# Optimization experiments

Measured on AMD Instinct MI355X. Metric: run time of the kernel, lower is better.

## Reference

```python
import jax, jax.numpy as jnp
import numpy as np
import math

B, C, HLAT, WLON = 1, 256, 46, 90
HEADS = 8
KC = 256   # k_channels (defaults to in_channels)
OC = 256   # out_channels (defaults to in_channels)


def _cc_weights(n):
    # Clenshaw-Curtis quadrature weights on n nodes x_k = cos(k*pi/(n-1)) over [-1, 1]
    # (torch-harmonics 'equiangular' grid quadrature); weights sum to 2.
    N = n - 1
    k = np.arange(n)
    j = np.arange(1, N // 2 + 1)
    b = np.where(2 * j == N, 1.0, 2.0)
    s = (b / (4.0 * j**2 - 1.0))[None, :] * np.cos(2.0 * np.pi * np.outer(k, j) / N)
    w = (1.0 - s.sum(axis=1)) * (2.0 / N)
    w[0] *= 0.5
    w[-1] *= 0.5
    return w


def _log_quad_weights(nlat, nlon):
    wgl = _cc_weights(nlat).astype(np.float32)            # [nlat]
    qw = 2.0 * np.pi * wgl / nlon                          # [nlat]
    qw = np.tile(qw.reshape(-1, 1), (1, nlon)).flatten()   # [nlat*nlon]
    return np.log(qw).reshape(1, 1, -1)                    # (1, 1, N)


def setup_inputs() -> dict:
    key = jax.random.key(0)
    ks = jax.random.split(key, 6)
    scale_qkv = math.sqrt(3.0 / C)
    scale_proj = math.sqrt(3.0 / OC)
    uni = lambda k, shp, s: s * (2.0 * jax.random.uniform(k, shp, dtype=jnp.float32) - 1.0)
    return {
        "query": jax.random.normal(ks[0], (B, C, HLAT, WLON), dtype=jnp.float32),
        "q_w": uni(ks[1], (KC, C), scale_qkv),
        "q_b": jnp.zeros((KC,), dtype=jnp.float32),
        "k_w": uni(ks[2], (KC, C), scale_qkv),
        "k_b": jnp.zeros((KC,), dtype=jnp.float32),
        "v_w": uni(ks[3], (OC, C), scale_qkv),
        "v_b": jnp.zeros((OC,), dtype=jnp.float32),
        "p_w": uni(ks[4], (OC, OC), scale_proj),
        "p_b": jnp.zeros((OC,), dtype=jnp.float32),
        "log_qw": jnp.asarray(_log_quad_weights(HLAT, WLON)),
    }


def _conv1x1(x, w, b):
    # 1x1 conv == per-pixel channel GEMM
    return jnp.einsum("bchw,kc->bkhw", x, w) + b[None, :, None, None]


def _to_seq(x, heads):
    # [B, heads*d, H, W] -> [B, heads, H*W, d]
    b, c, h, w = x.shape
    d = c // heads
    return x.reshape(b, heads, d, h, w).transpose(0, 1, 3, 4, 2).reshape(b, heads, h * w, d)


def reference(query, q_w, q_b, k_w, k_b, v_w, v_b, p_w, p_b, log_qw):
    # key = value = query (self-attention path of the module)
    q = _conv1x1(query, q_w, q_b)
    k = _conv1x1(query, k_w, k_b)
    v = _conv1x1(query, v_w, v_b)

    qs = _to_seq(q, HEADS)   # [B, h, N, dk]
    ks = _to_seq(k, HEADS)   # [B, h, M, dk]
    vs = _to_seq(v, HEADS)   # [B, h, M, dv]

    dk = KC // HEADS
    scale = 1.0 / math.sqrt(dk)  # SDPA default scale
    # scores with additive log-quadrature-weight bias over keys
    scores = jnp.einsum("bhnd,bhmd->bhnm", qs, ks) * scale + log_qw[:, :, None, :]
    attn = jax.nn.softmax(scores, axis=-1)
    out = jnp.einsum("bhnm,bhmd->bhnd", attn, vs)  # [B, h, N, dv]

    bb, hh, nn, dv = out.shape
    out = out.transpose(0, 1, 3, 2).reshape(bb, hh * dv, HLAT, WLON)
    out = _conv1x1(out, p_w, p_b)
    return out
```

## Files before the change

### kernel.cpp

```cpp
#include <hip/hip_runtime.h>

#define N_SEQ 4140
#define NP    4160
#define C_IN  256
#define HEADS 8
#define NT32  130
#define HN    (HEADS * N_SEQ)
#define LOG2E 1.4426950408889634f
#define SCALE2 (0.17677669529663687f * LOG2E)
#define INVSCALE 5.656854249492381f

typedef _Float16 f16x8 __attribute__((ext_vector_type(8)));
typedef float    f32x16 __attribute__((ext_vector_type(16)));

__device__ inline unsigned short f16b(float x) {
    union { _Float16 h; unsigned short s; } c;
    c.h = (_Float16)x;
    return c.s;
}
__device__ inline unsigned pack2h(float lo, float hi) {
    union { _Float16 h[2]; unsigned u; } c;
    c.h[0] = (_Float16)lo;
    c.h[1] = (_Float16)hi;
    return c.u;
}
__device__ inline void permswap(unsigned &a, unsigned &b) {
    asm volatile("v_permlane32_swap_b32 %0, %1" : "+v"(a), "+v"(b));
}

__global__ __launch_bounds__(256) void prep_kernel(
    const float* __restrict__ x, const float* __restrict__ log_qw,
    const float* __restrict__ q_w, const float* __restrict__ k_w,
    const float* __restrict__ v_w, const float* __restrict__ p_w,
    unsigned short* __restrict__ xt, float* __restrict__ lw2,
    unsigned short* __restrict__ wf, unsigned short* __restrict__ pwf)
{
    if (blockIdx.x < NT32) {
        __shared__ unsigned short tile[32][33];
        const int tx = threadIdx.x & 31, ty = threadIdx.x >> 5;
        const int n0 = blockIdx.x * 32, c0 = blockIdx.y * 32;
#pragma unroll
        for (int i = 0; i < 4; ++i) {
            const int c = c0 + ty * 4 + i;
            const int n = n0 + tx;
            const float v = (n < N_SEQ) ? x[(size_t)c * N_SEQ + n] : 0.f;
            tile[tx][ty * 4 + i] = f16b(v);
        }
        __syncthreads();
#pragma unroll
        for (int i = 0; i < 4; ++i) {
            const int nl = ty * 4 + i;
            xt[(size_t)(n0 + nl) * C_IN + c0 + tx] = tile[nl][tx];
        }
    } else {
        const int bid = (blockIdx.x - NT32) * 8 + blockIdx.y;
        for (int i = bid * 256 + threadIdx.x; i < 262144 + NP; i += 24 * 256) {
            if (i < 65536)        wf[i] = f16b(q_w[i]);
            else if (i < 131072)  wf[i] = f16b(k_w[i - 65536]);
            else if (i < 196608)  wf[i] = f16b(v_w[i - 131072]);
            else if (i < 262144)  pwf[i - 196608] = f16b(p_w[i - 196608]);
            else {
                const int j = i - 262144;
                lw2[j] = (j < N_SEQ) ? log_qw[j] * INVSCALE : -1e30f;
            }
        }
    }
}

__global__ __launch_bounds__(256) void qkv_mfma(
    const unsigned short* __restrict__ xt, const unsigned short* __restrict__ wf,
    const float* __restrict__ q_b, const float* __restrict__ k_b,
    const float* __restrict__ v_b,
    unsigned short* __restrict__ qo, unsigned short* __restrict__ ko,
    unsigned short* __restrict__ vo)
{
    const int tid = threadIdx.x, wid = tid >> 6, lane = tid & 63;
    const int col = lane & 31, hi = lane >> 5;
    const int w = blockIdx.x * 4 + wid;
    const int ot = w / 65, pt = w % 65;
    const int n0 = pt * 64, n1 = n0 + 32;

    if (ot < 16) {
        const unsigned short* a0 = xt + (size_t)(n0 + col) * C_IN + hi * 8;
        const unsigned short* a1 = xt + (size_t)(n1 + col) * C_IN + hi * 8;
        const unsigned short* bw = wf + (size_t)(ot * 32 + col) * C_IN + hi * 8;
        const float bias = (ot < 8) ? q_b[ot * 32 + col] : k_b[(ot - 8) * 32 + col];
        f32x16 acc0, acc1;
#pragma unroll
        for (int r = 0; r < 16; ++r) { acc0[r] = bias; acc1[r] = bias; }
#pragma unroll
        for (int t = 0; t < 16; ++t) {
            const f16x8 bf  = *(const f16x8*)(const void*)(bw + t * 16);
            const f16x8 af0 = *(const f16x8*)(const void*)(a0 + t * 16);
            const f16x8 af1 = *(const f16x8*)(const void*)(a1 + t * 16);
            acc0 = __builtin_amdgcn_mfma_f32_32x32x16_f16(af0, bf, acc0, 0, 0, 0);
            acc1 = __builtin_amdgcn_mfma_f32_32x32x16_f16(af1, bf, acc1, 0, 0, 0);
        }
        unsigned short* dst = (ot < 8) ? qo : ko;
        const int h = ot & 7;
#pragma unroll
        for (int r = 0; r < 16; ++r) {
            const int rl = (r & 3) + 8 * (r >> 2) + 4 * hi;
            dst[(size_t)(h * NP + n0 + rl) * 32 + col] = f16b(acc0[r]);
            dst[(size_t)(h * NP + n1 + rl) * 32 + col] = f16b(acc1[r]);
        }
    } else {
        const int h = ot - 16;
        const unsigned short* aw = wf + (size_t)(512 + h * 32 + col) * C_IN + hi * 8;
        const unsigned short* b0 = xt + (size_t)(n0 + col) * C_IN + hi * 8;
        const unsigned short* b1 = xt + (size_t)(n1 + col) * C_IN + hi * 8;
        const float* vb4 = v_b + h * 32 + 4 * hi;
        const float4 c0 = *(const float4*)(vb4);
        const float4 c1 = *(const float4*)(vb4 + 8);
        const float4 c2 = *(const float4*)(vb4 + 16);
        const float4 c3 = *(const float4*)(vb4 + 24);
        f32x16 acc0;
        acc0[0]=c0.x; acc0[1]=c0.y; acc0[2]=c0.z; acc0[3]=c0.w;
        acc0[4]=c1.x; acc0[5]=c1.y; acc0[6]=c1.z; acc0[7]=c1.w;
        acc0[8]=c2.x; acc0[9]=c2.y; acc0[10]=c2.z; acc0[11]=c2.w;
        acc0[12]=c3.x; acc0[13]=c3.y; acc0[14]=c3.z; acc0[15]=c3.w;
        f32x16 acc1 = acc0;
#pragma unroll
        for (int t = 0; t < 16; ++t) {
            const f16x8 af  = *(const f16x8*)(const void*)(aw + t * 16);
            const f16x8 bf0 = *(const f16x8*)(const void*)(b0 + t * 16);
            const f16x8 bf1 = *(const f16x8*)(const void*)(b1 + t * 16);
            acc0 = __builtin_amdgcn_mfma_f32_32x32x16_f16(af, bf0, acc0, 0, 0, 0);
            acc1 = __builtin_amdgcn_mfma_f32_32x32x16_f16(af, bf1, acc1, 0, 0, 0);
        }
        const int nt0 = pt * 2, nt1 = nt0 + 1;
#pragma unroll
        for (int r = 0; r < 16; ++r) {
            const int d = (r & 3) + 8 * (r >> 2) + 4 * hi;
            vo[((size_t)(h * NT32 + nt0) * 32 + d) * 32 + col] = f16b(acc0[r]);
            vo[((size_t)(h * NT32 + nt1) * 32 + d) * 32 + col] = f16b(acc1[r]);
        }
    }
}

__global__ __launch_bounds__(256) void attn_mfma_kernel(
    const unsigned short* __restrict__ qb, const unsigned short* __restrict__ kb,
    const unsigned short* __restrict__ vb, const float* __restrict__ lw2,
    float* __restrict__ pm, float* __restrict__ pl, float* __restrict__ pacc,
    int tiles_per_z)
{
    const int tid = threadIdx.x;
    const int wid = tid >> 6;
    const int lane = tid & 63;
    const int col = lane & 31;
    const int hi = lane >> 5;
    const int job = blockIdx.x * 4 + wid;
    const int h = job / 65;
    const int pt = job % 65;
    const int z = blockIdx.y;

    const int qrowA = pt * 64 + col;
    const int qrowB = qrowA + 32;
    const unsigned short* qpA = qb + ((size_t)(h * NP + qrowA)) * 32 + hi * 8;
    const unsigned short* qpB = qb + ((size_t)(h * NP + qrowB)) * 32 + hi * 8;
    const f16x8 qfA0 = *(const f16x8*)(const void*)(qpA);
    const f16x8 qfA1 = *(const f16x8*)(const void*)(qpA + 16);
    const f16x8 qfB0 = *(const f16x8*)(const void*)(qpB);
    const f16x8 qfB1 = *(const f16x8*)(const void*)(qpB + 16);

    f32x16 oA, oB;
#pragma unroll
    for (int r = 0; r < 16; ++r) { oA[r] = 0.f; oB[r] = 0.f; }
    float mA = -1e30f, lsA = 0.f;
    float mB = -1e30f, lsB = 0.f;

    const int t0 = z * tiles_per_z;
    const int t1 = min(NT32, t0 + tiles_per_z);
    const unsigned short* kbase = kb + (size_t)h * NP * 32;
    const unsigned short* vbase = vb + (size_t)h * NT32 * 1024;

    for (int t = t0; t < t1; ++t) {
        const int k0 = t * 32;
        const unsigned short* kp = kbase + (size_t)(k0 + col) * 32 + hi * 8;
        const f16x8 ka0 = *(const f16x8*)(const void*)(kp);
        const f16x8 ka1 = *(const f16x8*)(const void*)(kp + 16);
        const unsigned short* vp = vbase + (size_t)t * 1024 + col * 32 + hi * 8;
        const f16x8 va0 = *(const f16x8*)(const void*)(vp);
        const f16x8 va1 = *(const f16x8*)(const void*)(vp + 16);

        const float* lw4 = lw2 + k0 + 4 * hi;
        const float4 w0 = *(const float4*)(lw4);
        const float4 w1 = *(const float4*)(lw4 + 8);
        const float4 w2 = *(const float4*)(lw4 + 16);
        const float4 w3 = *(const float4*)(lw4 + 24);
        f32x16 sI;
        sI[0]=w0.x; sI[1]=w0.y; sI[2]=w0.z; sI[3]=w0.w;
        sI[4]=w1.x; sI[5]=w1.y; sI[6]=w1.z; sI[7]=w1.w;
        sI[8]=w2.x; sI[9]=w2.y; sI[10]=w2.z; sI[11]=w2.w;
        sI[12]=w3.x; sI[13]=w3.y; sI[14]=w3.z; sI[15]=w3.w;

        f32x16 sA = sI, sB = sI;
        sA = __builtin_amdgcn_mfma_f32_32x32x16_f16(ka0, qfA0, sA, 0, 0, 0);
        sB = __builtin_amdgcn_mfma_f32_32x32x16_f16(ka0, qfB0, sB, 0, 0, 0);
        sA = __builtin_amdgcn_mfma_f32_32x32x16_f16(ka1, qfA1, sA, 0, 0, 0);
        sB = __builtin_amdgcn_mfma_f32_32x32x16_f16(ka1, qfB1, sB, 0, 0, 0);

        float pA[16], pB[16];
#pragma unroll
        for (int r = 0; r < 16; ++r) { pA[r] = sA[r] * SCALE2; pB[r] = sB[r] * SCALE2; }

        float ax0 = fmaxf(pA[0], pA[1]),   ax1 = fmaxf(pA[2], pA[3]);
        float ax2 = fmaxf(pA[4], pA[5]),   ax3 = fmaxf(pA[6], pA[7]);
        float ax4 = fmaxf(pA[8], pA[9]),   ax5 = fmaxf(pA[10], pA[11]);
        float ax6 = fmaxf(pA[12], pA[13]), ax7 = fmaxf(pA[14], pA[15]);
        float bx0 = fmaxf(pB[0], pB[1]),   bx1 = fmaxf(pB[2], pB[3]);
        float bx2 = fmaxf(pB[4], pB[5]),   bx3 = fmaxf(pB[6], pB[7]);
        float bx4 = fmaxf(pB[8], pB[9]),   bx5 = fmaxf(pB[10], pB[11]);
        float bx6 = fmaxf(pB[12], pB[13]), bx7 = fmaxf(pB[14], pB[15]);
        ax0 = fmaxf(ax0, ax1); ax2 = fmaxf(ax2, ax3);
        ax4 = fmaxf(ax4, ax5); ax6 = fmaxf(ax6, ax7);
        bx0 = fmaxf(bx0, bx1); bx2 = fmaxf(bx2, bx3);
        bx4 = fmaxf(bx4, bx5); bx6 = fmaxf(bx6, bx7);
        const float cmaxA = fmaxf(fmaxf(ax0, ax2), fmaxf(ax4, ax6));
        const float cmaxB = fmaxf(fmaxf(bx0, bx2), fmaxf(bx4, bx6));

        if (!__all(cmaxA - mA <= 8.0f)) {
            float cw = fmaxf(cmaxA, __shfl_xor(cmaxA, 32));
            const float mnew = fmaxf(mA, cw);
            const float esc = __builtin_amdgcn_exp2f(mA - mnew);
            lsA *= esc;
#pragma unroll
            for (int r = 0; r < 16; ++r) oA[r] *= esc;
            mA = mnew;
        }
        if (!__all(cmaxB - mB <= 8.0f)) {
            float cw = fmaxf(cmaxB, __shfl_xor(cmaxB, 32));
            const float mnew = fmaxf(mB, cw);
            const float esc = __builtin_amdgcn_exp2f(mB - mnew);
            lsB *= esc;
#pragma unroll
            for (int r = 0; r < 16; ++r) oB[r] *= esc;
            mB = mnew;
        }

#pragma unroll
        for (int r = 0; r < 16; ++r) {
            pA[r] = __builtin_amdgcn_exp2f(pA[r] - mA);
            pB[r] = __builtin_amdgcn_exp2f(pB[r] - mB);
        }
        {
            float s0 = (pA[0] + pA[1]) + (pA[2] + pA[3]);
            float s1 = (pA[4] + pA[5]) + (pA[6] + pA[7]);
            float s2 = (pA[8] + pA[9]) + (pA[10] + pA[11]);
            float s3 = (pA[12] + pA[13]) + (pA[14] + pA[15]);
            lsA += (s0 + s1) + (s2 + s3);
            float u0 = (pB[0] + pB[1]) + (pB[2] + pB[3]);
            float u1 = (pB[4] + pB[5]) + (pB[6] + pB[7]);
            float u2 = (pB[8] + pB[9]) + (pB[10] + pB[11]);
            float u3 = (pB[12] + pB[13]) + (pB[14] + pB[15]);
            lsB += (u0 + u1) + (u2 + u3);
        }

        union U { unsigned u[4]; f16x8 v; };
        {
            unsigned a0 = pack2h(pA[0], pA[1]),  b0 = pack2h(pA[2], pA[3]);
            unsigned c0 = pack2h(pA[4], pA[5]),  d0 = pack2h(pA[6], pA[7]);
            permswap(a0, c0); permswap(b0, d0);
            U pb0; pb0.u[0]=a0; pb0.u[1]=b0; pb0.u[2]=c0; pb0.u[3]=d0;
            oA = __builtin_amdgcn_mfma_f32_32x32x16_f16(va0, pb0.v, oA, 0, 0, 0);
            unsigned e0 = pack2h(pA[8], pA[9]),   f0 = pack2h(pA[10], pA[11]);
            unsigned g0 = pack2h(pA[12], pA[13]), h0 = pack2h(pA[14], pA[15]);
            permswap(e0, g0); permswap(f0, h0);
            U pb1; pb1.u[0]=e0; pb1.u[1]=f0; pb1.u[2]=g0; pb1.u[3]=h0;
            oA = __builtin_amdgcn_mfma_f32_32x32x16_f16(va1, pb1.v, oA, 0, 0, 0);
        }
        {
            unsigned a0 = pack2h(pB[0], pB[1]),  b0 = pack2h(pB[2], pB[3]);
            unsigned c0 = pack2h(pB[4], pB[5]),  d0 = pack2h(pB[6], pB[7]);
            permswap(a0, c0); permswap(b0, d0);
            U pb0; pb0.u[0]=a0; pb0.u[1]=b0; pb0.u[2]=c0; pb0.u[3]=d0;
            oB = __builtin_amdgcn_mfma_f32_32x32x16_f16(va0, pb0.v, oB, 0, 0, 0);
            unsigned e0 = pack2h(pB[8], pB[9]),   f0 = pack2h(pB[10], pB[11]);
            unsigned g0 = pack2h(pB[12], pB[13]), h0 = pack2h(pB[14], pB[15]);
            permswap(e0, g0); permswap(f0, h0);
            U pb1; pb1.u[0]=e0; pb1.u[1]=f0; pb1.u[2]=g0; pb1.u[3]=h0;
            oB = __builtin_amdgcn_mfma_f32_32x32x16_f16(va1, pb1.v, oB, 0, 0, 0);
        }
    }

    lsA += __shfl_xor(lsA, 32);
    lsB += __shfl_xor(lsB, 32);

    if (qrowA < N_SEQ) {
        const size_t qi = (size_t)h * N_SEQ + qrowA;
        if (hi == 0) {
            pm[(size_t)z * HN + qi] = mA;
            pl[(size_t)z * HN + qi] = lsA;
        }
        float* pa = pacc + ((size_t)z * HN + qi) * 32;
#pragma unroll
        for (int r = 0; r < 16; ++r)
            pa[(r & 3) + 8 * (r >> 2) + 4 * hi] = oA[r];
    }
    if (qrowB < N_SEQ) {
        const size_t qi = (size_t)h * N_SEQ + qrowB;
        if (hi == 0) {
            pm[(size_t)z * HN + qi] = mB;
            pl[(size_t)z * HN + qi] = lsB;
        }
        float* pa = pacc + ((size_t)z * HN + qi) * 32;
#pragma unroll
        for (int r = 0; r < 16; ++r)
            pa[(r & 3) + 8 * (r >> 2) + 4 * hi] = oB[r];
    }
}

__global__ __launch_bounds__(256) void merge_kernel(
    const float* __restrict__ pm, const float* __restrict__ pl,
    const float* __restrict__ pacc, unsigned short* __restrict__ at_t, int nz)
{
    const int idx = blockIdx.x * 256 + threadIdx.x;
    if (idx >= HN) return;
    const int h = idx / N_SEQ;
    const int n = idx - h * N_SEQ;

    float mg = pm[idx];
    for (int zz = 1; zz < nz; ++zz) mg = fmaxf(mg, pm[(size_t)zz * HN + idx]);

    float lg = 0.f;
    float acc[32];
#pragma unroll
    for (int d = 0; d < 32; ++d) acc[d] = 0.f;
    for (int zz = 0; zz < nz; ++zz) {
        const float e = exp2f(pm[(size_t)zz * HN + idx] - mg);
        lg += pl[(size_t)zz * HN + idx] * e;
        const float* pa = pacc + ((size_t)zz * HN + idx) * 32;
#pragma unroll
        for (int d = 0; d < 32; ++d) acc[d] = fmaf(pa[d], e, acc[d]);
    }
    const float inv = 1.0f / lg;
    union { unsigned short s[32]; uint4 u[4]; } ph;
#pragma unroll
    for (int d = 0; d < 32; ++d) ph.s[d] = f16b(acc[d] * inv);
    uint4* dst = (uint4*)(at_t + (size_t)n * C_IN + h * 32);
#pragma unroll
    for (int i = 0; i < 4; ++i) dst[i] = ph.u[i];
}

__global__ __launch_bounds__(256) void proj_mfma(
    const unsigned short* __restrict__ at_t, const unsigned short* __restrict__ pwf,
    const float* __restrict__ p_b, float* __restrict__ out)
{
    const int tid = threadIdx.x, wid = tid >> 6, lane = tid & 63;
    const int col = lane & 31, hi = lane >> 5;
    const int tile = blockIdx.x * 4 + wid;
    const int ot = tile / NT32, nt = tile % NT32;
    const int n0 = nt * 32;

    const unsigned short* arow = pwf + (size_t)(ot * 32 + col) * C_IN + hi * 8;
    const unsigned short* brow = at_t + (size_t)(n0 + col) * C_IN + hi * 8;

    const float* pb4 = p_b + ot * 32 + 4 * hi;
    const float4 c0 = *(const float4*)(pb4);
    const float4 c1 = *(const float4*)(pb4 + 8);
    const float4 c2 = *(const float4*)(pb4 + 16);
    const float4 c3 = *(const float4*)(pb4 + 24);
    f32x16 acca, accb;
    acca[0]=c0.x; acca[1]=c0.y; acca[2]=c0.z; acca[3]=c0.w;
    acca[4]=c1.x; acca[5]=c1.y; acca[6]=c1.z; acca[7]=c1.w;
    acca[8]=c2.x; acca[9]=c2.y; acca[10]=c2.z; acca[11]=c2.w;
    acca[12]=c3.x; acca[13]=c3.y; acca[14]=c3.z; acca[15]=c3.w;
#pragma unroll
    for (int r = 0; r < 16; ++r) accb[r] = 0.f;

#pragma unroll
    for (int t = 0; t < 8; ++t) {
        const f16x8 afa = *(const f16x8*)(const void*)(arow + t * 16);
        const f16x8 bfa = *(const f16x8*)(const void*)(brow + t * 16);
        const f16x8 afb = *(const f16x8*)(const void*)(arow + (t + 8) * 16);
        const f16x8 bfb = *(const f16x8*)(const void*)(brow + (t + 8) * 16);
        acca = __builtin_amdgcn_mfma_f32_32x32x16_f16(afa, bfa, acca, 0, 0, 0);
        accb = __builtin_amdgcn_mfma_f32_32x32x16_f16(afb, bfb, accb, 0, 0, 0);
    }

    const int n = n0 + col;
    if (n < N_SEQ) {
#pragma unroll
        for (int r = 0; r < 16; ++r) {
            const int oc = ot * 32 + (r & 3) + 8 * (r >> 2) + 4 * hi;
            out[(size_t)oc * N_SEQ + n] = acca[r] + accb[r];
        }
    }
}

extern "C" void kernel_launch(void* const* d_in, const int* in_sizes, int n_in,
                              void* d_out, int out_size, void* d_ws, size_t ws_size,
                              hipStream_t stream) {
    const float* query  = (const float*)d_in[0];
    const float* q_w    = (const float*)d_in[1];
    const float* q_b    = (const float*)d_in[2];
    const float* k_w    = (const float*)d_in[3];
    const float* k_b    = (const float*)d_in[4];
    const float* v_w    = (const float*)d_in[5];
    const float* v_b    = (const float*)d_in[6];
    const float* p_w    = (const float*)d_in[7];
    const float* p_b    = (const float*)d_in[8];
    const float* log_qw = (const float*)d_in[9];

    const size_t HNP32 = (size_t)HEADS * NP * 32;

    unsigned short* xt  = (unsigned short*)d_ws;
    unsigned short* qb  = xt + (size_t)NP * C_IN;
    unsigned short* kb  = qb + HNP32;
    unsigned short* vb  = kb + HNP32;
    unsigned short* wf  = vb + HNP32;
    unsigned short* pwf = wf + 768 * 256;
    float* lw2 = (float*)(pwf + 256 * 256);
    float* pm  = lw2 + NP;
    unsigned short* at_t = qb;

    const size_t base_bytes = (size_t)((char*)pm - (char*)d_ws);
    const size_t per_z = (size_t)HN * 34 * sizeof(float);
    int nz = 1;
    if      (ws_size >= base_bytes + 4 * per_z) nz = 4;
    else if (ws_size >= base_bytes + 2 * per_z) nz = 2;
    const int tiles_per_z = (NT32 + nz - 1) / nz;

    float* pl   = pm + (size_t)nz * HN;
    float* pacc = pl + (size_t)nz * HN;

    prep_kernel<<<dim3(NT32 + 3, 8), 256, 0, stream>>>(
        query, log_qw, q_w, k_w, v_w, p_w, xt, lw2, wf, pwf);

    qkv_mfma<<<dim3(390), 256, 0, stream>>>(
        xt, wf, q_b, k_b, v_b, qb, kb, vb);

    attn_mfma_kernel<<<dim3(130, nz), 256, 0, stream>>>(
        qb, kb, vb, lw2, pm, pl, pacc, tiles_per_z);

    merge_kernel<<<dim3((HN + 255) / 256), 256, 0, stream>>>(
        pm, pl, pacc, at_t, nz);

    proj_mfma<<<dim3(260), 256, 0, stream>>>(
        at_t, pwf, p_b, (float*)d_out);
}
```

Baseline: 181.0 us.

## Fold softmax scale into Q weights, use packed f16 convert and dot2 row sums

Pre-multiplies the Q projection weights and bias by the log2-scaled softmax factor and stores the bias as log_qw*LOG2E, which removes the per-element score scaling in the attention inner loop. Converts probabilities with cvt_pkrtz and computes row sums with fdot2 on the packed f16 values, replacing separate float adds and per-half conversions. Also allows an 8-way key split when the workspace is large enough, giving more blocks in exchange for a larger merge step. Row sums now come from round-toward-zero f16 values, which slightly changes precision.

Result: faster. 171.6 us (-5.2%).

```diff
diff --git a/kernel.cpp b/kernel.cpp
--- a/kernel.cpp
+++ b/kernel.cpp
@@ -8,9 +8,9 @@
 #define HN    (HEADS * N_SEQ)
 #define LOG2E 1.4426950408889634f
 #define SCALE2 (0.17677669529663687f * LOG2E)
-#define INVSCALE 5.656854249492381f
 
 typedef _Float16 f16x8 __attribute__((ext_vector_type(8)));
+typedef _Float16 f16x2 __attribute__((ext_vector_type(2)));
 typedef float    f32x16 __attribute__((ext_vector_type(16)));
 
 __device__ inline unsigned short f16b(float x) {
@@ -18,11 +18,11 @@
     c.h = (_Float16)x;
     return c.s;
 }
-__device__ inline unsigned pack2h(float lo, float hi) {
-    union { _Float16 h[2]; unsigned u; } c;
-    c.h[0] = (_Float16)lo;
-    c.h[1] = (_Float16)hi;
-    return c.u;
+__device__ inline f16x2 pkrtz(float a, float b) {
+    auto r = __builtin_amdgcn_cvt_pkrtz(a, b);
+    union { decltype(r) i; f16x2 o; } c;
+    c.i = r;
+    return c.o;
 }
 __device__ inline void permswap(unsigned &a, unsigned &b) {
     asm volatile("v_permlane32_swap_b32 %0, %1" : "+v"(a), "+v"(b));
@@ -55,13 +55,13 @@
     } else {
         const int bid = (blockIdx.x - NT32) * 8 + blockIdx.y;
         for (int i = bid * 256 + threadIdx.x; i < 262144 + NP; i += 24 * 256) {
-            if (i < 65536)        wf[i] = f16b(q_w[i]);
+            if (i < 65536)        wf[i] = f16b(q_w[i] * SCALE2);
             else if (i < 131072)  wf[i] = f16b(k_w[i - 65536]);
             else if (i < 196608)  wf[i] = f16b(v_w[i - 131072]);
             else if (i < 262144)  pwf[i - 196608] = f16b(p_w[i - 196608]);
             else {
                 const int j = i - 262144;
-                lw2[j] = (j < N_SEQ) ? log_qw[j] * INVSCALE : -1e30f;
+                lw2[j] = (j < N_SEQ) ? log_qw[j] * LOG2E : -1e30f;
             }
         }
     }
@@ -84,7 +84,8 @@
         const unsigned short* a0 = xt + (size_t)(n0 + col) * C_IN + hi * 8;
         const unsigned short* a1 = xt + (size_t)(n1 + col) * C_IN + hi * 8;
         const unsigned short* bw = wf + (size_t)(ot * 32 + col) * C_IN + hi * 8;
-        const float bias = (ot < 8) ? q_b[ot * 32 + col] : k_b[(ot - 8) * 32 + col];
+        const float bias = (ot < 8) ? q_b[ot * 32 + col] * SCALE2
+                                    : k_b[(ot - 8) * 32 + col];
         f32x16 acc0, acc1;
 #pragma unroll
         for (int r = 0; r < 16; ++r) { acc0[r] = bias; acc1[r] = bias; }
@@ -168,6 +169,7 @@
     for (int r = 0; r < 16; ++r) { oA[r] = 0.f; oB[r] = 0.f; }
     float mA = -1e30f, lsA = 0.f;
     float mB = -1e30f, lsB = 0.f;
+    const f16x2 one2 = { (_Float16)1.f, (_Float16)1.f };
 
     const int t0 = z * tiles_per_z;
     const int t1 = min(NT32, t0 + tiles_per_z);
@@ -188,36 +190,32 @@
         const float4 w1 = *(const float4*)(lw4 + 8);
         const float4 w2 = *(const float4*)(lw4 + 16);
         const float4 w3 = *(const float4*)(lw4 + 24);
-        f32x16 sI;
-        sI[0]=w0.x; sI[1]=w0.y; sI[2]=w0.z; sI[3]=w0.w;
-        sI[4]=w1.x; sI[5]=w1.y; sI[6]=w1.z; sI[7]=w1.w;
-        sI[8]=w2.x; sI[9]=w2.y; sI[10]=w2.z; sI[11]=w2.w;
-        sI[12]=w3.x; sI[13]=w3.y; sI[14]=w3.z; sI[15]=w3.w;
-
-        f32x16 sA = sI, sB = sI;
+        f32x16 sA;
+        sA[0]=w0.x; sA[1]=w0.y; sA[2]=w0.z; sA[3]=w0.w;
+        sA[4]=w1.x; sA[5]=w1.y; sA[6]=w1.z; sA[7]=w1.w;
+        sA[8]=w2.x; sA[9]=w2.y; sA[10]=w2.z; sA[11]=w2.w;
+        sA[12]=w3.x; sA[13]=w3.y; sA[14]=w3.z; sA[15]=w3.w;
+        f32x16 sB = sA;
+
         sA = __builtin_amdgcn_mfma_f32_32x32x16_f16(ka0, qfA0, sA, 0, 0, 0);
         sB = __builtin_amdgcn_mfma_f32_32x32x16_f16(ka0, qfB0, sB, 0, 0, 0);
         sA = __builtin_amdgcn_mfma_f32_32x32x16_f16(ka1, qfA1, sA, 0, 0, 0);
         sB = __builtin_amdgcn_mfma_f32_32x32x16_f16(ka1, qfB1, sB, 0, 0, 0);
 
-        float pA[16], pB[16];
-#pragma unroll
-        for (int r = 0; r < 16; ++r) { pA[r] = sA[r] * SCALE2; pB[r] = sB[r] * SCALE2; }
-
-        float ax0 = fmaxf(pA[0], pA[1]),   ax1 = fmaxf(pA[2], pA[3]);
-        float ax2 = fmaxf(pA[4], pA[5]),   ax3 = fmaxf(pA[6], pA[7]);
-        float ax4 = fmaxf(pA[8], pA[9]),   ax5 = fmaxf(pA[10], pA[11]);
-        float ax6 = fmaxf(pA[12], pA[13]), ax7 = fmaxf(pA[14], pA[15]);
-        float bx0 = fmaxf(pB[0], pB[1]),   bx1 = fmaxf(pB[2], pB[3]);
-        float bx2 = fmaxf(pB[4], pB[5]),   bx3 = fmaxf(pB[6], pB[7]);
-        float bx4 = fmaxf(pB[8], pB[9]),   bx5 = fmaxf(pB[10], pB[11]);
-        float bx6 = fmaxf(pB[12], pB[13]), bx7 = fmaxf(pB[14], pB[15]);
-        ax0 = fmaxf(ax0, ax1); ax2 = fmaxf(ax2, ax3);
-        ax4 = fmaxf(ax4, ax5); ax6 = fmaxf(ax6, ax7);
-        bx0 = fmaxf(bx0, bx1); bx2 = fmaxf(bx2, bx3);
-        bx4 = fmaxf(bx4, bx5); bx6 = fmaxf(bx6, bx7);
-        const float cmaxA = fmaxf(fmaxf(ax0, ax2), fmaxf(ax4, ax6));
-        const float cmaxB = fmaxf(fmaxf(bx0, bx2), fmaxf(bx4, bx6));
+        const float a0m = fmaxf(fmaxf(sA[0], sA[1]), sA[2]);
+        const float a1m = fmaxf(fmaxf(sA[3], sA[4]), sA[5]);
+        const float a2m = fmaxf(fmaxf(sA[6], sA[7]), sA[8]);
+        const float a3m = fmaxf(fmaxf(sA[9], sA[10]), sA[11]);
+        const float a4m = fmaxf(fmaxf(sA[12], sA[13]), sA[14]);
+        const float cmaxA = fmaxf(fmaxf(fmaxf(a0m, a1m), a2m),
+                                  fmaxf(fmaxf(a3m, a4m), sA[15]));
+        const float b0m = fmaxf(fmaxf(sB[0], sB[1]), sB[2]);
+        const float b1m = fmaxf(fmaxf(sB[3], sB[4]), sB[5]);
+        const float b2m = fmaxf(fmaxf(sB[6], sB[7]), sB[8]);
+        const float b3m = fmaxf(fmaxf(sB[9], sB[10]), sB[11]);
+        const float b4m = fmaxf(fmaxf(sB[12], sB[13]), sB[14]);
+        const float cmaxB = fmaxf(fmaxf(fmaxf(b0m, b1m), b2m),
+                                  fmaxf(fmaxf(b3m, b4m), sB[15]));
 
         if (!__all(cmaxA - mA <= 8.0f)) {
             float cw = fmaxf(cmaxA, __shfl_xor(cmaxA, 32));
@@ -238,48 +236,65 @@
             mB = mnew;
         }
 
+        float pA[16], pB[16];
 #pragma unroll
         for (int r = 0; r < 16; ++r) {
-            pA[r] = __builtin_amdgcn_exp2f(pA[r] - mA);
-            pB[r] = __builtin_amdgcn_exp2f(pB[r] - mB);
-        }
+            pA[r] = __builtin_amdgcn_exp2f(sA[r] - mA);
+            pB[r] = __builtin_amdgcn_exp2f(sB[r] - mB);
+        }
+
+        union PK { f16x2 h[4]; unsigned u[4]; f16x8 v; };
         {
-            float s0 = (pA[0] + pA[1]) + (pA[2] + pA[3]);
-            float s1 = (pA[4] + pA[5]) + (pA[6] + pA[7]);
-            float s2 = (pA[8] + pA[9]) + (pA[10] + pA[11]);
-            float s3 = (pA[12] + pA[13]) + (pA[14] + pA[15]);
-            lsA += (s0 + s1) + (s2 + s3);
-            float u0 = (pB[0] + pB[1]) + (pB[2] + pB[3]);
-            float u1 = (pB[4] + pB[5]) + (pB[6] + pB[7]);
-            float u2 = (pB[8] + pB[9]) + (pB[10] + pB[11]);
-            float u3 = (pB[12] + pB[13]) + (pB[14] + pB[15]);
-            lsB += (u0 + u1) + (u2 + u3);
-        }
-
-        union U { unsigned u[4]; f16x8 v; };
+            PK k0p, k1p;
+            k0p.h[0] = pkrtz(pA[0], pA[1]);
+            k0p.h[1] = pkrtz(pA[2], pA[3]);
+            k0p.h[2] = pkrtz(pA[4], pA[5]);
+            k0p.h[3] = pkrtz(pA[6], pA[7]);
+            k1p.h[0] = pkrtz(pA[8], pA[9]);
+            k1p.h[1] = pkrtz(pA[10], pA[11]);
+            k1p.h[2] = pkrtz(pA[12], pA[13]);
+            k1p.h[3] = pkrtz(pA[14], pA[15]);
+            float sa = __builtin_amdgcn_fdot2(k0p.h[0], one2, 0.f, false);
+            float sb = __builtin_amdgcn_fdot2(k0p.h[1], one2, 0.f, false);
+            sa = __builtin_amdgcn_fdot2(k0p.h[2], one2, sa, false);
+            sb = __builtin_amdgcn_fdot2(k0p.h[3], one2, sb, false);
+            sa = __builtin_amdgcn_fdot2(k1p.h[0], one2, sa, false);
+            sb = __builtin_amdgcn_fdot2(k1p.h[1], one2, sb, false);
+            sa = __builtin_amdgcn_fdot2(k1p.h[2], one2, sa, false);
+            sb = __builtin_amdgcn_fdot2(k1p.h[3], one2, sb, false);
+            lsA += sa + sb;
+            permswap(k0p.u[0], k0p.u[2]);
+            permswap(k0p.u[1], k0p.u[3]);
+            oA = __builtin_amdgcn_mfma_f32_32x32x16_f16(va0, k0p.v, oA, 0, 0, 0);
+            permswap(k1p.u[0], k1p.u[2]);
+            permswap(k1p.u[1], k1p.u[3]);
+            oA = __builtin_amdgcn_mfma_f32_32x32x16_f16(va1, k1p.v, oA, 0, 0, 0);
+        }
         {
-            unsigned a0 = pack2h(pA[0], pA[1]),  b0 = pack2h(pA[2], pA[3]);
-            unsigned c0 = pack2h(pA[4], pA[5]),  d0 = pack2h(pA[6], pA[7]);
-            permswap(a0, c0); permswap(b0, d0);
-            U pb0; pb0.u[0]=a0; pb0.u[1]=b0; pb0.u[2]=c0; pb0.u[3]=d0;
-            oA = __builtin_amdgcn_mfma_f32_32x32x16_f16(va0, pb0.v, oA, 0, 0, 0);
-            unsigned e0 = pack2h(pA[8], pA[9]),   f0 = pack2h(pA[10], pA[11]);
-            unsigned g0 = pack2h(pA[12], pA[13]), h0 = pack2h(pA[14], pA[15]);
-            permswap(e0, g0); permswap(f0, h0);
-            U pb1; pb1.u[0]=e0; pb1.u[1]=f0; pb1.u[2]=g0; pb1.u[3]=h0;
-            oA = __builtin_amdgcn_mfma_f32_32x32x16_f16(va1, pb1.v, oA, 0, 0, 0);
-        }
-        {
-            unsigned a0 = pack2h(pB[0], pB[1]),  b0 = pack2h(pB[2], pB[3]);
-            unsigned c0 = pack2h(pB[4], pB[5]),  d0 = pack2h(pB[6], pB[7]);
-            permswap(a0, c0); permswap(b0, d0);
-            U pb0; pb0.u[0]=a0; pb0.u[1]=b0; pb0.u[2]=c0; pb0.u[3]=d0;
-            oB = __builtin_amdgcn_mfma_f32_32x32x16_f16(va0, pb0.v, oB, 0, 0, 0);
-            unsigned e0 = pack2h(pB[8], pB[9]),   f0 = pack2h(pB[10], pB[11]);
-            unsigned g0 = pack2h(pB[12], pB[13]), h0 = pack2h(pB[14], pB[15]);
-            permswap(e0, g0); permswap(f0, h0);
-            U pb1; pb1.u[0]=e0; pb1.u[1]=f0; pb1.u[2]=g0; pb1.u[3]=h0;
-            oB = __builtin_amdgcn_mfma_f32_32x32x16_f16(va1, pb1.v, oB, 0, 0, 0);
+            PK k0p, k1p;
+            k0p.h[0] = pkrtz(pB[0], pB[1]);
+            k0p.h[1] = pkrtz(pB[2], pB[3]);
+            k0p.h[2] = pkrtz(pB[4], pB[5]);
+            k0p.h[3] = pkrtz(pB[6], pB[7]);
+            k1p.h[0] = pkrtz(pB[8], pB[9]);
+            k1p.h[1] = pkrtz(pB[10], pB[11]);
+            k1p.h[2] = pkrtz(pB[12], pB[13]);
+            k1p.h[3] = pkrtz(pB[14], pB[15]);
+            float sa = __builtin_amdgcn_fdot2(k0p.h[0], one2, 0.f, false);
+            float sb = __builtin_amdgcn_fdot2(k0p.h[1], one2, 0.f, false);
+            sa = __builtin_amdgcn_fdot2(k0p.h[2], one2, sa, false);
+            sb = __builtin_amdgcn_fdot2(k0p.h[3], one2, sb, false);
+            sa = __builtin_amdgcn_fdot2(k1p.h[0], one2, sa, false);
+            sb = __builtin_amdgcn_fdot2(k1p.h[1], one2, sb, false);
+            sa = __builtin_amdgcn_fdot2(k1p.h[2], one2, sa, false);
+            sb = __builtin_amdgcn_fdot2(k1p.h[3], one2, sb, false);
+            lsB += sa + sb;
+            permswap(k0p.u[0], k0p.u[2]);
+            permswap(k0p.u[1], k0p.u[3]);
+            oB = __builtin_amdgcn_mfma_f32_32x32x16_f16(va0, k0p.v, oB, 0, 0, 0);
+            permswap(k1p.u[0], k1p.u[2]);
+            permswap(k1p.u[1], k1p.u[3]);
+            oB = __builtin_amdgcn_mfma_f32_32x32x16_f16(va1, k1p.v, oB, 0, 0, 0);
         }
     }
 
@@ -417,7 +432,8 @@
     const size_t base_bytes = (size_t)((char*)pm - (char*)d_ws);
     const size_t per_z = (size_t)HN * 34 * sizeof(float);
     int nz = 1;
-    if      (ws_size >= base_bytes + 4 * per_z) nz = 4;
+    if      (ws_size >= base_bytes + 8 * per_z) nz = 8;
+    else if (ws_size >= base_bytes + 4 * per_z) nz = 4;
     else if (ws_size >= base_bytes + 2 * per_z) nz = 2;
     const int tiles_per_z = (NT32 + nz - 1) / nz;
 
```
